# Optimization experiments

Measured on AMD Instinct MI355X. Metric: run time of the kernel, lower is better.

The kernel has to match this reference:

```python
import jax, jax.numpy as jnp
import numpy as np

# Dimensions (see shape_source): 28 indices per sample, values in [0, 8)
NX, NY, DIM, VOCAB = 2048, 2048, 28, 8
INTRA, INTER = 1.0, 2.0  # intra_class_distance, inter_class_distance
NCLS = 3
# index -> class id, derived from set_list = [[3,4,5,6],[0,1,2],[7]]
LUT = jnp.array([1, 1, 1, 0, 0, 0, 0, 2], dtype=jnp.int32)


def setup_inputs() -> dict:
    key = jax.random.key(0)
    k1, k2 = jax.random.split(key)
    return {
        "set_r": jax.random.randint(k1, (NX, DIM), 0, VOCAB, dtype=jnp.int32),
        "set_t": jax.random.randint(k2, (NY, DIM), 0, VOCAB, dtype=jnp.int32),
        "sigma": jnp.ones((), dtype=jnp.float32),
    }


def reference(set_r, set_t, sigma):
    # Per-position distance rule (from vector_distance, since set_list covers
    # every index exactly once):
    #   r == t                -> 0
    #   class(r) == class(t)  -> INTRA
    #   otherwise             -> INTER
    # sum over positions = INTRA*(cls_eq_cnt - eq_cnt) + INTER*(DIM - cls_eq_cnt)
    # Counts of matching positions are computed as one-hot GEMMs to avoid a
    # [NX, NY, DIM] intermediate.
    oh_r = jax.nn.one_hot(set_r, VOCAB, dtype=jnp.float32)       # [NX, DIM, V]
    oh_t = jax.nn.one_hot(set_t, VOCAB, dtype=jnp.float32)       # [NY, DIM, V]
    eq_cnt = jnp.einsum('idv,jdv->ij', oh_r, oh_t)               # [NX, NY]
    ch_r = jax.nn.one_hot(LUT[set_r], NCLS, dtype=jnp.float32)   # [NX, DIM, C]
    ch_t = jax.nn.one_hot(LUT[set_t], NCLS, dtype=jnp.float32)   # [NY, DIM, C]
    cls_cnt = jnp.einsum('idc,jdc->ij', ch_r, ch_t)              # [NX, NY]
    dist = (INTRA * (cls_cnt - eq_cnt) + INTER * (DIM - cls_cnt)) / DIM
    # Gaussain_kernel: exp(-d^2 / (2*sigma^2))
    return jnp.exp(-(dist ** 2) / (2.0 * sigma ** 2))
```

## Files before the change

kernel.cpp:

```cpp
#include <hip/hip_runtime.h>
#include <stdint.h>

#define NXD 2048
#define NYD 2048
#define DIMD 28
#define ROW_DW 12

#define CLS_TABLE 0x20000111u


__global__ __launch_bounds__(256) void pack_kernel(
    const int* __restrict__ set_r, const int* __restrict__ set_t,
    uint32_t* __restrict__ ws)
{
    const int row = blockIdx.x * 256 + threadIdx.x;
    const int* src = (row < NXD) ? (set_r + row * DIMD)
                                 : (set_t + (size_t)(row - NXD) * DIMD);
    int vals[DIMD];
    const int4* s4 = (const int4*)src;
    #pragma unroll
    for (int q = 0; q < 7; ++q) {
        int4 v = s4[q];
        vals[4*q+0] = v.x; vals[4*q+1] = v.y;
        vals[4*q+2] = v.z; vals[4*q+3] = v.w;
    }

    unsigned long long e0 = 0, e1 = 0, e2 = 0, e3 = 0;
    unsigned long long c0 = 0, c1 = 0;
    #pragma unroll
    for (int d = 0; d < DIMD; ++d) {
        const int v = vals[d];
        const int be = d * 8 + v;
        const unsigned long long bit = 1ull << (be & 63);
        switch (be >> 6) {
            case 0: e0 |= bit; break;
            case 1: e1 |= bit; break;
            case 2: e2 |= bit; break;
            default: e3 |= bit; break;
        }
        const int c = (CLS_TABLE >> (4 * v)) & 0xF;
        const int bc = d * 3 + c;
        if (bc < 64) c0 |= 1ull << bc;
        else         c1 |= 1ull << (bc - 64);
    }

    uint32_t w0 = (uint32_t)e0, w1 = (uint32_t)(e0 >> 32);
    uint32_t w2 = (uint32_t)e1, w3 = (uint32_t)(e1 >> 32);
    uint32_t w4 = (uint32_t)e2, w5 = (uint32_t)(e2 >> 32);
    uint32_t w6 = (uint32_t)e3;
    uint32_t w7 = (uint32_t)c0, w8 = (uint32_t)(c0 >> 32);
    uint32_t w9 = (uint32_t)c1;

    uint4* dst = (uint4*)(ws + (size_t)row * ROW_DW);
    dst[0] = make_uint4(w0, w1, w2, w3);
    dst[1] = make_uint4(w4, w5, w6, w7);
    dst[2] = make_uint4(w8, w9, 0u, 0u);
}

__global__ __launch_bounds__(256) void dist_kernel(
    const uint32_t* __restrict__ ws, const float* __restrict__ sigma_p,
    float* __restrict__ out)
{
    const int lane = threadIdx.x & 63;
    const int wave = threadIdx.x >> 6;
    const int i_base = blockIdx.y * 32 + wave * 8;
    const int j_base = blockIdx.x * 256 + lane * 4;

    const uint4* tp = (const uint4*)(ws + (size_t)(NXD + j_base) * ROW_DW);
    uint4 T[4][3];
    #pragma unroll
    for (int s = 0; s < 4; ++s) {
        T[s][0] = tp[s*3 + 0];
        T[s][1] = tp[s*3 + 1];
        T[s][2] = tp[s*3 + 2];
    }

    const float sg = sigma_p[0];
    const float k = 1.0f / (2.0f * sg * sg * (float)(DIMD * DIMD));

    const uint4* rp = (const uint4*)ws;
    #pragma unroll
    for (int ii = 0; ii < 8; ++ii) {
        const int i = i_base + ii;
        const uint4 R0 = rp[i*3 + 0];
        const uint4 R1 = rp[i*3 + 1];
        const uint4 R2 = rp[i*3 + 2];
        float4 res;
        #pragma unroll
        for (int s = 0; s < 4; ++s) {
            const int sum =
                __popc(R0.x & T[s][0].x) + __popc(R0.y & T[s][0].y) +
                __popc(R0.z & T[s][0].z) + __popc(R0.w & T[s][0].w) +
                __popc(R1.x & T[s][1].x) + __popc(R1.y & T[s][1].y) +
                __popc(R1.z & T[s][1].z) + __popc(R1.w & T[s][1].w) +
                __popc(R2.x & T[s][2].x) + __popc(R2.y & T[s][2].y);
            const float c = (float)(56 - sum);
            (&res.x)[s] = __expf(-c * c * k);
        }
        *(float4*)(out + (size_t)i * NYD + j_base) = res;
    }
}

extern "C" void kernel_launch(void* const* d_in, const int* in_sizes, int n_in,
                              void* d_out, int out_size, void* d_ws, size_t ws_size,
                              hipStream_t stream) {
    const int*   set_r = (const int*)d_in[0];
    const int*   set_t = (const int*)d_in[1];
    const float* sigma = (const float*)d_in[2];
    float*       out   = (float*)d_out;
    uint32_t*    ws    = (uint32_t*)d_ws;

    pack_kernel<<<dim3((NXD + NYD) / 256), dim3(256), 0, stream>>>(set_r, set_t, ws);

    dist_kernel<<<dim3(NYD / 256, NXD / 32), dim3(256), 0, stream>>>(ws, sigma, out);
}
```

Before: 73.20 us.

## Fuse row packing into distance kernel using shared-memory packed tiles

New measurement: 67.45 us. 1.09x faster.

```diff
diff --git a/kernel.cpp b/kernel.cpp
--- a/kernel.cpp
+++ b/kernel.cpp
@@ -4,89 +4,95 @@
 #define NXD 2048
 #define NYD 2048
 #define DIMD 28
-#define ROW_DW 12
-
 #define CLS_TABLE 0x20000111u
 
-
-__global__ __launch_bounds__(256) void pack_kernel(
-    const int* __restrict__ set_r, const int* __restrict__ set_t,
-    uint32_t* __restrict__ ws)
-{
-    const int row = blockIdx.x * 256 + threadIdx.x;
-    const int* src = (row < NXD) ? (set_r + row * DIMD)
-                                 : (set_t + (size_t)(row - NXD) * DIMD);
+__device__ __forceinline__ void pack_row(const int* __restrict__ src,
+                                         uint32_t* __restrict__ w ) {
     int vals[DIMD];
     const int4* s4 = (const int4*)src;
-    #pragma unroll
+#pragma unroll
     for (int q = 0; q < 7; ++q) {
-        int4 v = s4[q];
-        vals[4*q+0] = v.x; vals[4*q+1] = v.y;
-        vals[4*q+2] = v.z; vals[4*q+3] = v.w;
+        int4 t = s4[q];
+        vals[4*q+0] = t.x; vals[4*q+1] = t.y;
+        vals[4*q+2] = t.z; vals[4*q+3] = t.w;
     }
-
-    unsigned long long e0 = 0, e1 = 0, e2 = 0, e3 = 0;
-    unsigned long long c0 = 0, c1 = 0;
-    #pragma unroll
+    unsigned long long e0=0, e1=0, e2=0, e3=0, c0=0, c1=0;
+#pragma unroll
     for (int d = 0; d < DIMD; ++d) {
         const int v = vals[d];
-        const int be = d * 8 + v;
-        const unsigned long long bit = 1ull << (be & 63);
-        switch (be >> 6) {
-            case 0: e0 |= bit; break;
-            case 1: e1 |= bit; break;
-            case 2: e2 |= bit; break;
-            default: e3 |= bit; break;
+        const unsigned long long eb = 1ull << (((d*8) & 63) + v);
+        if      (d < 8)  e0 |= eb;
+        else if (d < 16) e1 |= eb;
+        else if (d < 24) e2 |= eb;
+        else             e3 |= eb;
+        const int c = (CLS_TABLE >> (4*v)) & 0xF;
+        if      (d*3 + 2 < 64) c0 |= 1ull << (d*3 + c);
+        else if (d*3 >= 64)    c1 |= 1ull << (d*3 - 64 + c);
+        else {
+            const unsigned long long b = 1ull << c;
+            c0 |= (b & 1ull) << 63;
+            c1 |= b >> 1;
         }
-        const int c = (CLS_TABLE >> (4 * v)) & 0xF;
-        const int bc = d * 3 + c;
-        if (bc < 64) c0 |= 1ull << bc;
-        else         c1 |= 1ull << (bc - 64);
     }
-
-    uint32_t w0 = (uint32_t)e0, w1 = (uint32_t)(e0 >> 32);
-    uint32_t w2 = (uint32_t)e1, w3 = (uint32_t)(e1 >> 32);
-    uint32_t w4 = (uint32_t)e2, w5 = (uint32_t)(e2 >> 32);
-    uint32_t w6 = (uint32_t)e3;
-    uint32_t w7 = (uint32_t)c0, w8 = (uint32_t)(c0 >> 32);
-    uint32_t w9 = (uint32_t)c1;
-
-    uint4* dst = (uint4*)(ws + (size_t)row * ROW_DW);
-    dst[0] = make_uint4(w0, w1, w2, w3);
-    dst[1] = make_uint4(w4, w5, w6, w7);
-    dst[2] = make_uint4(w8, w9, 0u, 0u);
+    w[0]=(uint32_t)e0; w[1]=(uint32_t)(e0>>32);
+    w[2]=(uint32_t)e1; w[3]=(uint32_t)(e1>>32);
+    w[4]=(uint32_t)e2; w[5]=(uint32_t)(e2>>32);
+    w[6]=(uint32_t)e3;
+    w[7]=(uint32_t)c0; w[8]=(uint32_t)(c0>>32);
+    w[9]=(uint32_t)c1;
+    w[10]=0u; w[11]=0u;
 }
 
-__global__ __launch_bounds__(256) void dist_kernel(
-    const uint32_t* __restrict__ ws, const float* __restrict__ sigma_p,
-    float* __restrict__ out)
+__global__ __launch_bounds__(256) void setdist_kernel(
+    const int* __restrict__ set_r, const int* __restrict__ set_t,
+    const float* __restrict__ sigma_p, float* __restrict__ out)
 {
-    const int lane = threadIdx.x & 63;
-    const int wave = threadIdx.x >> 6;
-    const int i_base = blockIdx.y * 32 + wave * 8;
-    const int j_base = blockIdx.x * 256 + lane * 4;
+    __shared__ uint32_t t_pk[256][12];
+    __shared__ uint32_t r_pk[32][12];
 
-    const uint4* tp = (const uint4*)(ws + (size_t)(NXD + j_base) * ROW_DW);
-    uint4 T[4][3];
-    #pragma unroll
-    for (int s = 0; s < 4; ++s) {
-        T[s][0] = tp[s*3 + 0];
-        T[s][1] = tp[s*3 + 1];
-        T[s][2] = tp[s*3 + 2];
+    const int tid = threadIdx.x;
+    const int i0 = blockIdx.y * 32;
+    const int j0 = blockIdx.x * 256;
+
+    {
+        uint32_t w[12];
+        pack_row(set_t + (size_t)(j0 + tid) * DIMD, w);
+        uint4* dst = (uint4*)t_pk[tid];
+        dst[0] = make_uint4(w[0], w[1], w[2], w[3]);
+        dst[1] = make_uint4(w[4], w[5], w[6], w[7]);
+        dst[2] = make_uint4(w[8], w[9], 0u, 0u);
+    }
+    if (tid < 32) {
+        uint32_t w[12];
+        pack_row(set_r + (size_t)(i0 + tid) * DIMD, w);
+        uint4* dst = (uint4*)r_pk[tid];
+        dst[0] = make_uint4(w[0], w[1], w[2], w[3]);
+        dst[1] = make_uint4(w[4], w[5], w[6], w[7]);
+        dst[2] = make_uint4(w[8], w[9], 0u, 0u);
     }
 
     const float sg = sigma_p[0];
     const float k = 1.0f / (2.0f * sg * sg * (float)(DIMD * DIMD));
 
-    const uint4* rp = (const uint4*)ws;
-    #pragma unroll
+    __syncthreads();
+
+    const int lane = tid & 63;
+    const int wave = tid >> 6;
+
+    uint4 T[4][3];
+#pragma unroll
+    for (int s = 0; s < 4; ++s) {
+        const uint4* tp = (const uint4*)t_pk[lane + 64*s];
+        T[s][0] = tp[0]; T[s][1] = tp[1]; T[s][2] = tp[2];
+    }
+
+    float* obase = out + (size_t)(i0 + wave * 8) * NYD + j0 + lane;
+
+#pragma unroll
     for (int ii = 0; ii < 8; ++ii) {
-        const int i = i_base + ii;
-        const uint4 R0 = rp[i*3 + 0];
-        const uint4 R1 = rp[i*3 + 1];
-        const uint4 R2 = rp[i*3 + 2];
-        float4 res;
-        #pragma unroll
+        const uint4* rp = (const uint4*)r_pk[wave * 8 + ii];
+        const uint4 R0 = rp[0], R1 = rp[1], R2 = rp[2];
+#pragma unroll
         for (int s = 0; s < 4; ++s) {
             const int sum =
                 __popc(R0.x & T[s][0].x) + __popc(R0.y & T[s][0].y) +
@@ -95,9 +101,8 @@
                 __popc(R1.z & T[s][1].z) + __popc(R1.w & T[s][1].w) +
                 __popc(R2.x & T[s][2].x) + __popc(R2.y & T[s][2].y);
             const float c = (float)(56 - sum);
-            (&res.x)[s] = __expf(-c * c * k);
+            obase[(size_t)ii * NYD + 64 * s] = __expf(-c * c * k);
         }
-        *(float4*)(out + (size_t)i * NYD + j_base) = res;
     }
 }
 
@@ -108,9 +113,7 @@
     const int*   set_t = (const int*)d_in[1];
     const float* sigma = (const float*)d_in[2];
     float*       out   = (float*)d_out;
-    uint32_t*    ws    = (uint32_t*)d_ws;
 
-    pack_kernel<<<dim3((NXD + NYD) / 256), dim3(256), 0, stream>>>(set_r, set_t, ws);
-
-    dist_kernel<<<dim3(NYD / 256, NXD / 32), dim3(256), 0, stream>>>(ws, sigma, out);
+    setdist_kernel<<<dim3(NYD / 256, NXD / 32), dim3(256), 0, stream>>>(
+        set_r, set_t, sigma, out);
 }
```
